# Optimization experiments

Hardware: AMD Instinct MI355X
Metric: run time of the kernel (lower is better)

## Reference

```python
import jax, jax.numpy as jnp
import numpy as np

D = 1024      # input_dim == attention_dim == num_heads*head_dim
H = 16        # num_heads
HD = 64       # head_dim
FF = 4096     # ff_dim
EPS = 1e-5


def _layernorm(x, gamma, beta):
    mu = jnp.mean(x, axis=-1, keepdims=True)
    var = jnp.var(x, axis=-1, keepdims=True)
    return (x - mu) * jax.lax.rsqrt(var + EPS) * gamma + beta


def setup_inputs() -> dict:
    key = jax.random.key(0)
    ks = jax.random.split(key, 11)
    s_in = 1.0 / np.sqrt(D)
    s_ff = 1.0 / np.sqrt(FF)
    return {
        "x": jax.random.normal(ks[0], (2, 2048, D), dtype=jnp.float32),
        "w_qkv": jax.random.uniform(ks[1], (D, 3 * D), jnp.float32, -s_in, s_in),
        "b_qkv": jax.random.uniform(ks[2], (3 * D,), jnp.float32, -s_in, s_in),
        "w_o": jax.random.uniform(ks[3], (D, D), jnp.float32, -s_in, s_in),
        "b_o": jax.random.uniform(ks[4], (D,), jnp.float32, -s_in, s_in),
        "g1": jnp.ones((D,), jnp.float32),
        "be1": jnp.zeros((D,), jnp.float32),
        "w1": jax.random.uniform(ks[5], (D, FF), jnp.float32, -s_in, s_in),
        "b1": jax.random.uniform(ks[6], (FF,), jnp.float32, -s_in, s_in),
        "w2": jax.random.uniform(ks[7], (FF, D), jnp.float32, -s_ff, s_ff),
        "b2": jax.random.uniform(ks[8], (D,), jnp.float32, -s_ff, s_ff),
        "g2": jnp.ones((D,), jnp.float32),
        "be2": jnp.zeros((D,), jnp.float32),
    }


def reference(x, w_qkv, b_qkv, w_o, b_o, g1, be1, w1, b1, w2, b2, g2, be2):
    N, L, _ = x.shape
    qkv = x @ w_qkv + b_qkv                       # [N, L, 3D]
    q = qkv[..., :D].reshape(N, L, H, HD)
    k = qkv[..., D:2 * D].reshape(N, L, H, HD)
    v = qkv[..., 2 * D:].reshape(N, L, H, HD)
    scores = jnp.einsum('nqhd,nkhd->nhqk', q, k) / np.sqrt(HD)
    attn = jax.nn.softmax(scores, axis=-1)        # [N, H, L, L]
    out = jnp.einsum('nhql,nlhd->nqhd', attn, v).reshape(N, L, D)
    attn_out = out @ w_o + b_o
    # dropout is identity in eval mode
    h = _layernorm(attn_out + x, g1, be1)
    ff = jax.nn.relu(h @ w1 + b1) @ w2 + b2
    return _layernorm(h + ff, g2, be2)
```

## Files before the change

### kernel.cpp

```cpp
#include <hip/hip_runtime.h>
#include <cstddef>
#include <cstdint>

static constexpr int Dm   = 1024;
static constexpr int Hh   = 16;
static constexpr int HDd  = 64;
static constexpr int FFd  = 4096;
static constexpr int Ls   = 2048;
static constexpr int Nb   = 2;
static constexpr int Mrows = Nb * Ls;

typedef short bf16x8 __attribute__((ext_vector_type(8)));
typedef float f32x4  __attribute__((ext_vector_type(4)));

__device__ __forceinline__ ushort f2b(float f) {
    uint32_t u = __builtin_bit_cast(uint32_t, f);
    u = (u + 0x7FFFu + ((u >> 16) & 1u)) >> 16;
    return (ushort)u;
}
__device__ __forceinline__ ushort f2bf(float f) {
    return (ushort)((__builtin_bit_cast(uint32_t, f) + 0x8000u) >> 16);
}
__device__ __forceinline__ float b2f(ushort b) {
    return __builtin_bit_cast(float, (uint32_t)b << 16);
}

__device__ __forceinline__ void gl2lds16(const ushort* g, ushort* l) {
    __builtin_amdgcn_global_load_lds(
        (const __attribute__((address_space(1))) void*)g,
        (__attribute__((address_space(3))) void*)l, 16, 0, 0);
}

__global__ __launch_bounds__(256) void convert_bf16(
    const float* __restrict__ src, ushort* __restrict__ dst, int n)
{
    int i = (blockIdx.x * 256 + threadIdx.x) * 4;
    if (i >= n) return;
    float4 v = *(const float4*)(src + i);
    uint2 o;
    o.x = (uint32_t)f2b(v.x) | ((uint32_t)f2b(v.y) << 16);
    o.y = (uint32_t)f2b(v.z) | ((uint32_t)f2b(v.w) << 16);
    *(uint2*)(dst + i) = o;
}

__global__ __launch_bounds__(256) void transpose_bf16(
    const float* __restrict__ src, ushort* __restrict__ dst, int K, int N)
{
    __shared__ float t[32][33];
    const int k0 = blockIdx.y * 32, n0 = blockIdx.x * 32;
    const int tx = threadIdx.x & 31, ty = threadIdx.x >> 5;
    #pragma unroll
    for (int i = 0; i < 4; ++i)
        t[ty + i * 8][tx] = src[(size_t)(k0 + ty + i * 8) * N + n0 + tx];
    __syncthreads();
    #pragma unroll
    for (int i = 0; i < 4; ++i)
        dst[(size_t)(n0 + ty + i * 8) * K + k0 + tx] = f2b(t[tx][ty + i * 8]);
}

template <int TN, int RELU, int VOUT>
__global__ __launch_bounds__(256) void gemm_mfma(
    const ushort* __restrict__ A, const ushort* __restrict__ Bt,
    const float* __restrict__ bias,
    ushort* __restrict__ Cb, ushort* __restrict__ vT, int M, int N, int K)
{
    constexpr int NT  = TN / 32;
    constexpr int BSZ = TN * 32;
    __shared__ __align__(16) ushort As[2 * 128 * 32];
    __shared__ __align__(16) ushort Bs[2 * BSZ];

    const int tid  = threadIdx.x;
    const int bm   = blockIdx.y * 128, bn = blockIdx.x * TN;
    const int wave = tid >> 6, lane = tid & 63;
    const int wm = (wave & 1) * 64;
    const int wn = (wave >> 1) * (TN / 2);
    const int lr = lane & 15, lq = lane >> 4;

    const int rr = wave * 16 + (lane >> 2);
    const int sg = lane & 3;
    const ushort* Ag = A  + (size_t)(bm + rr) * K + sg * 8;
    const ushort* Bg = Bt + (size_t)(bn + rr) * K + sg * 8;

    f32x4 acc[4][NT];
    #pragma unroll
    for (int i = 0; i < 4; ++i)
        #pragma unroll
        for (int j = 0; j < NT; ++j)
            acc[i][j] = (f32x4){0.f, 0.f, 0.f, 0.f};

    gl2lds16(Ag,                  As + wave * 512);
    gl2lds16(Ag + (size_t)64 * K, As + 2048 + wave * 512);
    gl2lds16(Bg,                  Bs + wave * 512);
    if (TN == 128)
        gl2lds16(Bg + (size_t)64 * K, Bs + 2048 + wave * 512);

    int ib = 0;
    for (int k0 = 0; k0 < K; k0 += 32, ib ^= 1) {
        __syncthreads();
        if (k0 + 32 < K) {
            const int nb = ib ^ 1;
            gl2lds16(Ag + k0 + 32,                  As + nb * 4096 + wave * 512);
            gl2lds16(Ag + k0 + 32 + (size_t)64 * K, As + nb * 4096 + 2048 + wave * 512);
            gl2lds16(Bg + k0 + 32,                  Bs + nb * BSZ + wave * 512);
            if (TN == 128)
                gl2lds16(Bg + k0 + 32 + (size_t)64 * K, Bs + nb * BSZ + 2048 + wave * 512);
        }

        const ushort* Ar = As + ib * 4096;
        const ushort* Br = Bs + ib * BSZ;
        bf16x8 af[4], bf[NT];
        #pragma unroll
        for (int mt = 0; mt < 4; ++mt)
            af[mt] = *(const bf16x8*)(Ar + (wm + mt * 16 + lr) * 32 + lq * 8);
        #pragma unroll
        for (int nt = 0; nt < NT; ++nt)
            bf[nt] = *(const bf16x8*)(Br + (wn + nt * 16 + lr) * 32 + lq * 8);

        #pragma unroll
        for (int mt = 0; mt < 4; ++mt)
            #pragma unroll
            for (int nt = 0; nt < NT; ++nt)
                acc[mt][nt] = __builtin_amdgcn_mfma_f32_16x16x32_bf16(
                    af[mt], bf[nt], acc[mt][nt], 0, 0, 0);
    }

    if (VOUT && bn >= 2 * Dm) {
        #pragma unroll
        for (int nt = 0; nt < NT; ++nt) {
            const int n = bn + wn + nt * 16 + lr;
            const float bv = bias[n];
            const int col = n - 2 * Dm;
            const int h = col >> 6, d = col & 63;
            #pragma unroll
            for (int mt = 0; mt < 4; ++mt) {
                const int m0 = bm + wm + mt * 16 + lq * 4;
                const int batch = m0 >> 11, key0 = m0 & (Ls - 1);
                ushort4 ob;
                ushort* op = (ushort*)&ob;
                #pragma unroll
                for (int r = 0; r < 4; ++r) op[r] = f2bf(acc[mt][nt][r] + bv);
                *(ushort4*)(vT + (((size_t)(batch * Hh + h)) * HDd + d) * Ls + key0) = ob;
            }
        }
        return;
    }
    #pragma unroll
    for (int nt = 0; nt < NT; ++nt) {
        const int n = bn + wn + nt * 16 + lr;
        const float bv = bias[n];
        #pragma unroll
        for (int mt = 0; mt < 4; ++mt) {
            const int m0 = bm + wm + mt * 16 + lq * 4;
            #pragma unroll
            for (int r = 0; r < 4; ++r) {
                float v = acc[mt][nt][r] + bv;
                if (RELU) v = fmaxf(v, 0.0f);
                Cb[(size_t)(m0 + r) * N + n] = f2bf(v);
            }
        }
    }
}

__global__ __launch_bounds__(256) void attn_mfma(
    const ushort* __restrict__ qkv, const ushort* __restrict__ vT,
    ushort* __restrict__ out)
{
    const int tid = threadIdx.x, wave = tid >> 6, lane = tid & 63;
    const int lr = lane & 15, lq = lane >> 4;
    const int h = blockIdx.y, n = blockIdx.z;
    const int q0 = blockIdx.x * 64 + wave * 16;
    const size_t RS = 3 * Dm;
    const ushort* base  = qkv + (size_t)n * Ls * RS;
    const ushort* vbase = vT + (size_t)(n * Hh + h) * HDd * Ls;

    __shared__ __align__(16) ushort Kb[64 * 72];
    __shared__ __align__(16) ushort Vt[64 * 72];
    __shared__ __align__(16) ushort Pq[4][16 * 72];

    bf16x8 qf[2];
    {
        const float c = 0.18033688011112042f;
        const ushort* qg = base + (size_t)(q0 + lr) * RS + h * HDd + lq * 8;
        bf16x8 t0 = *(const bf16x8*)(qg);
        bf16x8 t1 = *(const bf16x8*)(qg + 32);
        #pragma unroll
        for (int j = 0; j < 8; ++j) {
            qf[0][j] = (short)f2b(b2f((ushort)t0[j]) * c);
            qf[1][j] = (short)f2b(b2f((ushort)t1[j]) * c);
        }
    }

    f32x4 o[4];
    #pragma unroll
    for (int dt = 0; dt < 4; ++dt) o[dt] = (f32x4){0.f, 0.f, 0.f, 0.f};
    float lpart = 0.f;

    const int srow = tid >> 2, ssg = tid & 3;
    const ushort* kg = base + (size_t)srow * RS + Dm + h * HDd;
    const ushort* vg = vbase + (size_t)srow * Ls;
    ushort* Pw = Pq[wave];

    for (int kt = 0; kt < Ls; kt += 64) {
        const ushort* kp = kg + (size_t)kt * RS;
        const ushort* vp = vg + kt;
        int4 ka = *(const int4*)(kp + ssg * 8);
        int4 kb = *(const int4*)(kp + (ssg + 4) * 8);
        int4 va = *(const int4*)(vp + ssg * 8);
        int4 vb = *(const int4*)(vp + (ssg + 4) * 8);

        __syncthreads();
        *(int4*)(Kb + srow * 72 + ssg * 8)       = ka;
        *(int4*)(Kb + srow * 72 + (ssg + 4) * 8) = kb;
        *(int4*)(Vt + srow * 72 + ssg * 8)       = va;
        *(int4*)(Vt + srow * 72 + (ssg + 4) * 8) = vb;
        __syncthreads();

        f32x4 s[4];
        #pragma unroll
        for (int mt = 0; mt < 4; ++mt) s[mt] = (f32x4){0.f, 0.f, 0.f, 0.f};
        #pragma unroll
        for (int ks = 0; ks < 2; ++ks)
            #pragma unroll
            for (int mt = 0; mt < 4; ++mt) {
                bf16x8 kf = *(const bf16x8*)(Kb + (mt * 16 + lr) * 72 + ks * 32 + lq * 8);
                s[mt] = __builtin_amdgcn_mfma_f32_16x16x32_bf16(kf, qf[ks], s[mt], 0, 0, 0);
            }

        ushort4 pb[4];
        #pragma unroll
        for (int mt = 0; mt < 4; ++mt) {
            ushort* pw = (ushort*)&pb[mt];
            #pragma unroll
            for (int r = 0; r < 4; ++r) {
                float p = exp2f(s[mt][r]);
                lpart += p;
                pw[r] = f2bf(p);
            }
        }

        #pragma unroll
        for (int mt = 0; mt < 4; ++mt)
            *(ushort4*)(Pw + lr * 72 + mt * 16 + lq * 4) = pb[mt];

        #pragma unroll
        for (int ks = 0; ks < 2; ++ks) {
            bf16x8 pf = *(const bf16x8*)(Pw + lr * 72 + ks * 32 + lq * 8);
            #pragma unroll
            for (int dt = 0; dt < 4; ++dt) {
                bf16x8 vf = *(const bf16x8*)(Vt + (dt * 16 + lr) * 72 + ks * 32 + lq * 8);
                o[dt] = __builtin_amdgcn_mfma_f32_16x16x32_bf16(vf, pf, o[dt], 0, 0, 0);
            }
        }
    }

    float lrun = lpart;
    lrun += __shfl_xor(lrun, 16);
    lrun += __shfl_xor(lrun, 32);

    const float inv = 1.0f / lrun;
    ushort* orow = out + (size_t)(n * Ls + q0 + lr) * Dm + h * HDd;
    #pragma unroll
    for (int dt = 0; dt < 4; ++dt) {
        ushort4 ob;
        ushort* op = (ushort*)&ob;
        #pragma unroll
        for (int r = 0; r < 4; ++r) op[r] = f2bf(o[dt][r] * inv);
        *(ushort4*)(orow + dt * 16 + lq * 4) = ob;
    }
}

template <int A_BF16, int B_BF16, int OUT_F32>
__global__ __launch_bounds__(256) void add_ln(
    const void* __restrict__ a, const void* __restrict__ b,
    const float* __restrict__ gamma, const float* __restrict__ beta,
    float* __restrict__ outf, ushort* __restrict__ outb)
{
    const int row = blockIdx.x;
    const int tid = threadIdx.x;

    float va[4], vb[4];
    if (A_BF16) {
        ushort4 u = ((const ushort4*)((const ushort*)a + (size_t)row * Dm))[tid];
        va[0] = b2f(u.x); va[1] = b2f(u.y); va[2] = b2f(u.z); va[3] = b2f(u.w);
    } else {
        float4 f = ((const float4*)((const float*)a + (size_t)row * Dm))[tid];
        va[0] = f.x; va[1] = f.y; va[2] = f.z; va[3] = f.w;
    }
    if (B_BF16) {
        ushort4 u = ((const ushort4*)((const ushort*)b + (size_t)row * Dm))[tid];
        vb[0] = b2f(u.x); vb[1] = b2f(u.y); vb[2] = b2f(u.z); vb[3] = b2f(u.w);
    } else {
        float4 f = ((const float4*)((const float*)b + (size_t)row * Dm))[tid];
        vb[0] = f.x; vb[1] = f.y; vb[2] = f.z; vb[3] = f.w;
    }
    float v[4] = {va[0] + vb[0], va[1] + vb[1], va[2] + vb[2], va[3] + vb[3]};

    float s  = v[0] + v[1] + v[2] + v[3];
    float sq = v[0]*v[0] + v[1]*v[1] + v[2]*v[2] + v[3]*v[3];

    __shared__ float red[8];
    #pragma unroll
    for (int off = 32; off > 0; off >>= 1) {
        s  += __shfl_down(s, off);
        sq += __shfl_down(sq, off);
    }
    const int wv = tid >> 6;
    if ((tid & 63) == 0) { red[wv] = s; red[4 + wv] = sq; }
    __syncthreads();
    s  = red[0] + red[1] + red[2] + red[3];
    sq = red[4] + red[5] + red[6] + red[7];

    const float mu  = s * (1.0f / Dm);
    const float var = sq * (1.0f / Dm) - mu * mu;
    const float inv = rsqrtf(var + 1e-5f);

    const float4 g  = ((const float4*)gamma)[tid];
    const float4 be = ((const float4*)beta)[tid];
    float ov[4];
    ov[0] = (v[0] - mu) * inv * g.x + be.x;
    ov[1] = (v[1] - mu) * inv * g.y + be.y;
    ov[2] = (v[2] - mu) * inv * g.z + be.z;
    ov[3] = (v[3] - mu) * inv * g.w + be.w;
    if (OUT_F32) {
        float4 o4 = {ov[0], ov[1], ov[2], ov[3]};
        ((float4*)(outf + (size_t)row * Dm))[tid] = o4;
    } else {
        uint2 ob;
        ob.x = (uint32_t)f2bf(ov[0]) | ((uint32_t)f2bf(ov[1]) << 16);
        ob.y = (uint32_t)f2bf(ov[2]) | ((uint32_t)f2bf(ov[3]) << 16);
        *(uint2*)(outb + (size_t)row * Dm + tid * 4) = ob;
    }
}

extern "C" void kernel_launch(void* const* d_in, const int* in_sizes, int n_in,
                              void* d_out, int out_size, void* d_ws, size_t ws_size,
                              hipStream_t stream)
{
    const float* x     = (const float*)d_in[0];
    const float* w_qkv = (const float*)d_in[1];
    const float* b_qkv = (const float*)d_in[2];
    const float* w_o   = (const float*)d_in[3];
    const float* b_o   = (const float*)d_in[4];
    const float* g1    = (const float*)d_in[5];
    const float* be1   = (const float*)d_in[6];
    const float* w1    = (const float*)d_in[7];
    const float* b1    = (const float*)d_in[8];
    const float* w2    = (const float*)d_in[9];
    const float* b2    = (const float*)d_in[10];
    const float* g2    = (const float*)d_in[11];
    const float* be2   = (const float*)d_in[12];
    float* out = (float*)d_out;

    char* p = (char*)d_ws;
    ushort* qkvb  = (ushort*)p;  p += (size_t)Mrows * 3 * Dm * 2;
    ushort* attnb = (ushort*)p;  p += (size_t)Mrows * Dm * 2;
    ushort* projb = (ushort*)p;  p += (size_t)Mrows * Dm * 2;
    ushort* hb    = (ushort*)p;  p += (size_t)Mrows * Dm * 2;
    ushort* ffb   = (ushort*)p;  p += (size_t)Mrows * FFd * 2;
    ushort* ff2b  = (ushort*)p;  p += (size_t)Mrows * Dm * 2;
    ushort* xb    = (ushort*)p;  p += (size_t)Mrows * Dm * 2;
    ushort* wqkvT = (ushort*)p;  p += (size_t)(3 * Dm) * Dm * 2;
    ushort* woT   = (ushort*)p;  p += (size_t)Dm * Dm * 2;
    ushort* w1T   = (ushort*)p;  p += (size_t)FFd * Dm * 2;
    ushort* w2T   = (ushort*)p;  p += (size_t)Dm * FFd * 2;
    ushort* vTg   = (ushort*)p;  p += (size_t)Mrows * Dm * 2;

    convert_bf16<<<dim3(Mrows * Dm / 1024), dim3(256), 0, stream>>>(x, xb, Mrows * Dm);
    transpose_bf16<<<dim3(3 * Dm / 32, Dm / 32), dim3(256), 0, stream>>>(w_qkv, wqkvT, Dm, 3 * Dm);
    transpose_bf16<<<dim3(Dm / 32, Dm / 32),     dim3(256), 0, stream>>>(w_o, woT, Dm, Dm);
    transpose_bf16<<<dim3(FFd / 32, Dm / 32),    dim3(256), 0, stream>>>(w1, w1T, Dm, FFd);
    transpose_bf16<<<dim3(Dm / 32, FFd / 32),    dim3(256), 0, stream>>>(w2, w2T, FFd, Dm);

    gemm_mfma<128, 0, 1><<<dim3(3 * Dm / 128, Mrows / 128), dim3(256), 0, stream>>>(
        xb, wqkvT, b_qkv, qkvb, vTg, Mrows, 3 * Dm, Dm);

    attn_mfma<<<dim3(Ls / 64, Hh, Nb), dim3(256), 0, stream>>>(qkvb, vTg, attnb);

    gemm_mfma<64, 0, 0><<<dim3(Dm / 64, Mrows / 128), dim3(256), 0, stream>>>(
        attnb, woT, b_o, projb, nullptr, Mrows, Dm, Dm);

    add_ln<1, 0, 0><<<dim3(Mrows), dim3(256), 0, stream>>>(projb, x, g1, be1, nullptr, hb);

    gemm_mfma<128, 1, 0><<<dim3(FFd / 128, Mrows / 128), dim3(256), 0, stream>>>(
        hb, w1T, b1, ffb, nullptr, Mrows, FFd, Dm);

    gemm_mfma<64, 0, 0><<<dim3(Dm / 64, Mrows / 128), dim3(256), 0, stream>>>(
        ffb, w2T, b2, ff2b, nullptr, Mrows, Dm, FFd);

    add_ln<1, 1, 1><<<dim3(Mrows), dim3(256), 0, stream>>>(ff2b, hb, g2, be2, out, nullptr);
}
```

Baseline: 413.6 us.

## Process 32 query rows per wave in attention and prefetch next K/V tile

Each wave of the attention kernel now handles two 16-row query slices, so every K and V fragment read from shared memory feeds two MFMAs and each block covers 128 queries. The grid is halved to match. The global loads for the next K/V tile are issued right after the shared-memory store, so they overlap with the current tile's compute. In exchange the kernel uses more registers and LDS per block and launches fewer blocks (512), which may lower occupancy.

```diff
diff --git a/kernel.cpp b/kernel.cpp
--- a/kernel.cpp
+++ b/kernel.cpp
@@ -168,46 +168,50 @@
     const int tid = threadIdx.x, wave = tid >> 6, lane = tid & 63;
     const int lr = lane & 15, lq = lane >> 4;
     const int h = blockIdx.y, n = blockIdx.z;
-    const int q0 = blockIdx.x * 64 + wave * 16;
+    const int q0 = blockIdx.x * 128 + wave * 32;
     const size_t RS = 3 * Dm;
     const ushort* base  = qkv + (size_t)n * Ls * RS;
     const ushort* vbase = vT + (size_t)(n * Hh + h) * HDd * Ls;
 
     __shared__ __align__(16) ushort Kb[64 * 72];
     __shared__ __align__(16) ushort Vt[64 * 72];
-    __shared__ __align__(16) ushort Pq[4][16 * 72];
-
-    bf16x8 qf[2];
+    __shared__ __align__(16) ushort Pq[4][32 * 72];
+
+    bf16x8 qf[2][2];
     {
         const float c = 0.18033688011112042f;
-        const ushort* qg = base + (size_t)(q0 + lr) * RS + h * HDd + lq * 8;
-        bf16x8 t0 = *(const bf16x8*)(qg);
-        bf16x8 t1 = *(const bf16x8*)(qg + 32);
-        #pragma unroll
-        for (int j = 0; j < 8; ++j) {
-            qf[0][j] = (short)f2b(b2f((ushort)t0[j]) * c);
-            qf[1][j] = (short)f2b(b2f((ushort)t1[j]) * c);
-        }
-    }
-
-    f32x4 o[4];
-    #pragma unroll
-    for (int dt = 0; dt < 4; ++dt) o[dt] = (f32x4){0.f, 0.f, 0.f, 0.f};
-    float lpart = 0.f;
+        #pragma unroll
+        for (int qh = 0; qh < 2; ++qh) {
+            const ushort* qg = base + (size_t)(q0 + qh * 16 + lr) * RS + h * HDd + lq * 8;
+            bf16x8 t0 = *(const bf16x8*)(qg);
+            bf16x8 t1 = *(const bf16x8*)(qg + 32);
+            #pragma unroll
+            for (int j = 0; j < 8; ++j) {
+                qf[0][qh][j] = (short)f2b(b2f((ushort)t0[j]) * c);
+                qf[1][qh][j] = (short)f2b(b2f((ushort)t1[j]) * c);
+            }
+        }
+    }
+
+    f32x4 o[4][2];
+    #pragma unroll
+    for (int dt = 0; dt < 4; ++dt)
+        #pragma unroll
+        for (int qh = 0; qh < 2; ++qh)
+            o[dt][qh] = (f32x4){0.f, 0.f, 0.f, 0.f};
+    float lpart[2] = {0.f, 0.f};
 
     const int srow = tid >> 2, ssg = tid & 3;
     const ushort* kg = base + (size_t)srow * RS + Dm + h * HDd;
     const ushort* vg = vbase + (size_t)srow * Ls;
     ushort* Pw = Pq[wave];
 
+    int4 ka = *(const int4*)(kg + ssg * 8);
+    int4 kb = *(const int4*)(kg + (ssg + 4) * 8);
+    int4 va = *(const int4*)(vg + ssg * 8);
+    int4 vb = *(const int4*)(vg + (ssg + 4) * 8);
+
     for (int kt = 0; kt < Ls; kt += 64) {
-        const ushort* kp = kg + (size_t)kt * RS;
-        const ushort* vp = vg + kt;
-        int4 ka = *(const int4*)(kp + ssg * 8);
-        int4 kb = *(const int4*)(kp + (ssg + 4) * 8);
-        int4 va = *(const int4*)(vp + ssg * 8);
-        int4 vb = *(const int4*)(vp + (ssg + 4) * 8);
-
         __syncthreads();
         *(int4*)(Kb + srow * 72 + ssg * 8)       = ka;
         *(int4*)(Kb + srow * 72 + (ssg + 4) * 8) = kb;
@@ -215,57 +219,84 @@
         *(int4*)(Vt + srow * 72 + (ssg + 4) * 8) = vb;
         __syncthreads();
 
-        f32x4 s[4];
-        #pragma unroll
-        for (int mt = 0; mt < 4; ++mt) s[mt] = (f32x4){0.f, 0.f, 0.f, 0.f};
+        if (kt + 64 < Ls) {
+            const ushort* kp = kg + (size_t)(kt + 64) * RS;
+            const ushort* vp = vg + (kt + 64);
+            ka = *(const int4*)(kp + ssg * 8);
+            kb = *(const int4*)(kp + (ssg + 4) * 8);
+            va = *(const int4*)(vp + ssg * 8);
+            vb = *(const int4*)(vp + (ssg + 4) * 8);
+        }
+
+        f32x4 s[4][2];
+        #pragma unroll
+        for (int mt = 0; mt < 4; ++mt)
+            #pragma unroll
+            for (int qh = 0; qh < 2; ++qh)
+                s[mt][qh] = (f32x4){0.f, 0.f, 0.f, 0.f};
         #pragma unroll
         for (int ks = 0; ks < 2; ++ks)
             #pragma unroll
             for (int mt = 0; mt < 4; ++mt) {
                 bf16x8 kf = *(const bf16x8*)(Kb + (mt * 16 + lr) * 72 + ks * 32 + lq * 8);
-                s[mt] = __builtin_amdgcn_mfma_f32_16x16x32_bf16(kf, qf[ks], s[mt], 0, 0, 0);
-            }
-
-        ushort4 pb[4];
-        #pragma unroll
-        for (int mt = 0; mt < 4; ++mt) {
-            ushort* pw = (ushort*)&pb[mt];
-            #pragma unroll
-            for (int r = 0; r < 4; ++r) {
-                float p = exp2f(s[mt][r]);
-                lpart += p;
-                pw[r] = f2bf(p);
-            }
-        }
-
+                #pragma unroll
+                for (int qh = 0; qh < 2; ++qh)
+                    s[mt][qh] = __builtin_amdgcn_mfma_f32_16x16x32_bf16(
+                        kf, qf[ks][qh], s[mt][qh], 0, 0, 0);
+            }
+
+        ushort4 pb[4][2];
         #pragma unroll
         for (int mt = 0; mt < 4; ++mt)
-            *(ushort4*)(Pw + lr * 72 + mt * 16 + lq * 4) = pb[mt];
+            #pragma unroll
+            for (int qh = 0; qh < 2; ++qh) {
+                ushort* pw = (ushort*)&pb[mt][qh];
+                #pragma unroll
+                for (int r = 0; r < 4; ++r) {
+                    float p = exp2f(s[mt][qh][r]);
+                    lpart[qh] += p;
+                    pw[r] = f2bf(p);
+                }
+            }
+
+        #pragma unroll
+        for (int qh = 0; qh < 2; ++qh)
+            #pragma unroll
+            for (int mt = 0; mt < 4; ++mt)
+                *(ushort4*)(Pw + (qh * 16 + lr) * 72 + mt * 16 + lq * 4) = pb[mt][qh];
 
         #pragma unroll
         for (int ks = 0; ks < 2; ++ks) {
-            bf16x8 pf = *(const bf16x8*)(Pw + lr * 72 + ks * 32 + lq * 8);
+            bf16x8 pf[2];
+            #pragma unroll
+            for (int qh = 0; qh < 2; ++qh)
+                pf[qh] = *(const bf16x8*)(Pw + (qh * 16 + lr) * 72 + ks * 32 + lq * 8);
             #pragma unroll
             for (int dt = 0; dt < 4; ++dt) {
                 bf16x8 vf = *(const bf16x8*)(Vt + (dt * 16 + lr) * 72 + ks * 32 + lq * 8);
-                o[dt] = __builtin_amdgcn_mfma_f32_16x16x32_bf16(vf, pf, o[dt], 0, 0, 0);
-            }
-        }
-    }
-
-    float lrun = lpart;
-    lrun += __shfl_xor(lrun, 16);
-    lrun += __shfl_xor(lrun, 32);
-
-    const float inv = 1.0f / lrun;
-    ushort* orow = out + (size_t)(n * Ls + q0 + lr) * Dm + h * HDd;
-    #pragma unroll
-    for (int dt = 0; dt < 4; ++dt) {
-        ushort4 ob;
-        ushort* op = (ushort*)&ob;
-        #pragma unroll
-        for (int r = 0; r < 4; ++r) op[r] = f2bf(o[dt][r] * inv);
-        *(ushort4*)(orow + dt * 16 + lq * 4) = ob;
+                #pragma unroll
+                for (int qh = 0; qh < 2; ++qh)
+                    o[dt][qh] = __builtin_amdgcn_mfma_f32_16x16x32_bf16(
+                        vf, pf[qh], o[dt][qh], 0, 0, 0);
+            }
+        }
+    }
+
+    #pragma unroll
+    for (int qh = 0; qh < 2; ++qh) {
+        float lrun = lpart[qh];
+        lrun += __shfl_xor(lrun, 16);
+        lrun += __shfl_xor(lrun, 32);
+        const float inv = 1.0f / lrun;
+        ushort* orow = out + (size_t)(n * Ls + q0 + qh * 16 + lr) * Dm + h * HDd;
+        #pragma unroll
+        for (int dt = 0; dt < 4; ++dt) {
+            ushort4 ob;
+            ushort* op = (ushort*)&ob;
+            #pragma unroll
+            for (int r = 0; r < 4; ++r) op[r] = f2bf(o[dt][qh][r] * inv);
+            *(ushort4*)(orow + dt * 16 + lq * 4) = ob;
+        }
     }
 }
 
@@ -374,7 +405,7 @@
     gemm_mfma<128, 0, 1><<<dim3(3 * Dm / 128, Mrows / 128), dim3(256), 0, stream>>>(
         xb, wqkvT, b_qkv, qkvb, vTg, Mrows, 3 * Dm, Dm);
 
-    attn_mfma<<<dim3(Ls / 64, Hh, Nb), dim3(256), 0, stream>>>(qkvb, vTg, attnb);
+    attn_mfma<<<dim3(Ls / 128, Hh, Nb), dim3(256), 0, stream>>>(qkvb, vTg, attnb);
 
     gemm_mfma<64, 0, 0><<<dim3(Dm / 64, Mrows / 128), dim3(256), 0, stream>>>(
         attnb, woT, b_o, projb, nullptr, Mrows, Dm, Dm);
```

New measurement: 410.5 us. About the same (-0.7%).
